# Kernel tuning notes

Measured on AMD Instinct MI355X. Metric: run time of the kernel, lower is better.

Reference implementation:

```python
import jax, jax.numpy as jnp
import numpy as np

N_GEN, N_LOAD, N_OR, N_EX = 10000, 20000, 35000, 35000
N = N_GEN + N_LOAD + N_OR + N_EX  # 100000 objects
E = 1_600_000                      # edges (avg degree 16)
H = 64                             # N_node_hidden
L_HID = 7                          # N_GCN_layers - 1
NEG = 0.1                          # LeakyReLU negative slope
WS = 0.05                          # weight scale


def setup_inputs() -> dict:
    key = jax.random.key(0)
    ks = jax.random.split(key, 32)
    f = lambda i, s: jax.random.normal(ks[i], s, jnp.float32)
    p = lambda i, s: WS * jax.random.normal(ks[i], s, jnp.float32)
    return {
        "x_gen": f(0, (N_GEN, 3)),
        "x_load": f(1, (N_LOAD, 3)),
        "x_or": f(2, (N_OR, 6)),
        "x_ex": f(3, (N_EX, 6)),
        "edge_index": jax.random.randint(ks[4], (2, E), 0, N, jnp.int32),
        "object_ptv": jnp.arange(N, dtype=jnp.int32),
        "W_gen1": p(5, (3, H)), "b_gen1": p(6, (H,)),
        "W_gen2": p(7, (H, H)), "b_gen2": p(8, (H,)),
        "W_load1": p(9, (3, H)), "b_load1": p(10, (H,)),
        "W_load2": p(11, (H, H)), "b_load2": p(12, (H,)),
        "W_or1": p(13, (6, H)), "b_or1": p(14, (H,)),
        "W_or2": p(15, (H, H)), "b_or2": p(16, (H,)),
        "W_ex1": p(17, (6, H)), "b_ex1": p(18, (H,)),
        "W_ex2": p(19, (H, H)), "b_ex2": p(20, (H,)),
        "Wl_h": p(21, (L_HID, H, H)),
        "Wr_h": p(22, (L_HID, H, H)),
        "b_h": p(23, (L_HID, H)),
        "Wl_last": p(24, (H, 1)),
        "Wr_last": p(25, (H, 1)),
        "b_last": p(26, (1,)),
    }


def _encode(x, W1, b1, W2, b2):
    h = jax.nn.leaky_relu(x @ W1 + b1, NEG)
    return jax.nn.leaky_relu(h @ W2 + b2, NEG)


def reference(x_gen, x_load, x_or, x_ex, edge_index, object_ptv,
              W_gen1, b_gen1, W_gen2, b_gen2,
              W_load1, b_load1, W_load2, b_load2,
              W_or1, b_or1, W_or2, b_or2,
              W_ex1, b_ex1, W_ex2, b_ex2,
              Wl_h, Wr_h, b_h, Wl_last, Wr_last, b_last):
    # per-object-type MLP encoders
    xg = _encode(x_gen, W_gen1, b_gen1, W_gen2, b_gen2)
    xl = _encode(x_load, W_load1, b_load1, W_load2, b_load2)
    xo = _encode(x_or, W_or1, b_or1, W_or2, b_or2)
    xe = _encode(x_ex, W_ex1, b_ex1, W_ex2, b_ex2)
    x = jnp.concatenate([xg, xl, xo, xe], axis=0)[object_ptv]  # [N, H]

    src, dst = edge_index[0], edge_index[1]

    def sage(h, Wl, Wr, b):
        # SAGEConv(aggr='add', root_weight=True): lin_l(sum_j h_j) + lin_r(h_i) + b
        agg = jax.ops.segment_sum(h[src], dst, num_segments=N)  # gather + scatter-add
        return agg @ Wl + h @ Wr + b

    def step(h, params):
        Wl, Wr, b = params
        return jax.nn.leaky_relu(sage(h, Wl, Wr, b), NEG), None

    x, _ = jax.lax.scan(step, x, (Wl_h, Wr_h, b_h))
    return jax.nn.sigmoid(sage(x, Wl_last, Wr_last, b_last))  # [N, 1]
```

## Files before the change

kernel.cpp:

```cpp
#include <hip/hip_runtime.h>
#include <math.h>

#define HD 64
#define NEGS 0.1f
#define CHUNK 2048
#define NPART 8

typedef unsigned short u16;
typedef unsigned int u32;

__device__ __forceinline__ float leaky(float v) { return v > 0.f ? v : NEGS * v; }

__device__ __forceinline__ u16 f2bf(float f) {
    union { float f; u32 u; } v; v.f = f;
    u32 r = v.u + 0x7FFFu + ((v.u >> 16) & 1u);
    return (u16)(r >> 16);
}
__device__ __forceinline__ float bf2f(u16 u) {
    union { u32 i; float f; } v; v.i = ((u32)u) << 16; return v.f;
}
__device__ __forceinline__ float bflo(u32 x) {
    union { u32 i; float f; } v; v.i = x << 16; return v.f;
}
__device__ __forceinline__ float bfhi(u32 x) {
    union { u32 i; float f; } v; v.i = x & 0xFFFF0000u; return v.f;
}
__device__ __forceinline__ u32 pack2(float a, float b) {
    return (u32)f2bf(a) | ((u32)f2bf(b) << 16);
}

__global__ void zero_i32(int* __restrict__ p, int n) {
    int i = blockIdx.x * blockDim.x + threadIdx.x;
    int stride = gridDim.x * blockDim.x;
    for (; i < n; i += stride) p[i] = 0;
}

template <int IN>
__global__ void encode_k(const float* __restrict__ x,
                         const float* __restrict__ W1, const float* __restrict__ b1,
                         const float* __restrict__ W2, const float* __restrict__ b2,
                         u16* __restrict__ out, int n) {
    __shared__ float sW2[HD * HD];
    for (int idx = threadIdx.x; idx < HD * HD; idx += blockDim.x) sW2[idx] = W2[idx];
    __syncthreads();
    int wave = threadIdx.x >> 6, lane = threadIdx.x & 63;
    int i = blockIdx.x * 4 + wave;
    if (i >= n) return;
    float h1 = b1[lane];
#pragma unroll
    for (int d = 0; d < IN; ++d) h1 += x[i * IN + d] * W1[d * HD + lane];
    h1 = leaky(h1);
    float h2 = b2[lane];
#pragma unroll
    for (int k = 0; k < HD; ++k) {
        float hk = __shfl(h1, k);
        h2 += hk * sW2[k * HD + lane];
    }
    out[i * HD + lane] = f2bf(leaky(h2));
}

__global__ void gather_bf(const u16* __restrict__ enc, const int* __restrict__ ptv,
                          u16* __restrict__ out, int n) {
    int idx = blockIdx.x * blockDim.x + threadIdx.x;
    int stride = gridDim.x * blockDim.x;
    int total = n * (HD / 8);
    for (; idx < total; idx += stride) {
        int i = idx >> 3, ch = idx & 7;
        ((uint4*)(out + (size_t)i * HD))[ch] =
            ((const uint4*)(enc + (size_t)ptv[i] * HD))[ch];
    }
}

__global__ void __launch_bounds__(256) hist_part(const int* __restrict__ dst,
                                                 int* __restrict__ counts,
                                                 int E_, int part_sz) {
    int part = blockIdx.x & (NPART - 1);
    int slice = blockIdx.x >> 3;
    int nslices = gridDim.x >> 3;
    int lo = part * part_sz, hi = lo + part_sz;
    for (int e = slice * blockDim.x + threadIdx.x; e < E_; e += nslices * blockDim.x) {
        int d = dst[e];
        if (d >= lo && d < hi) atomicAdd(&counts[d], 1);
    }
}

__global__ void scan1(const int* __restrict__ counts, int* __restrict__ bsum, int n) {
    __shared__ int s[256];
    int b = blockIdx.x, t = threadIdx.x;
    int base = b * CHUNK + t * 8;
    int sum = 0;
#pragma unroll
    for (int u = 0; u < 8; ++u) {
        int i = base + u;
        if (i < n) sum += counts[i];
    }
    s[t] = sum;
    __syncthreads();
    for (int off = 128; off > 0; off >>= 1) {
        if (t < off) s[t] += s[t + off];
        __syncthreads();
    }
    if (t == 0) bsum[b] = s[0];
}

__global__ void scan2(int* __restrict__ bsum, int nb, int* __restrict__ row_ptr, int n) {
    if (threadIdx.x == 0 && blockIdx.x == 0) {
        int run = 0;
        for (int b = 0; b < nb; ++b) {
            int v = bsum[b];
            bsum[b] = run;
            run += v;
        }
        row_ptr[n] = run;
    }
}

__global__ void scan3(const int* __restrict__ counts, const int* __restrict__ bsum,
                      int* __restrict__ row_ptr, int* __restrict__ pos, int n) {
    __shared__ int s[256];
    int b = blockIdx.x, t = threadIdx.x;
    int base = b * CHUNK + t * 8;
    int c[8];
    int sum = 0;
#pragma unroll
    for (int u = 0; u < 8; ++u) {
        int i = base + u;
        c[u] = (i < n) ? counts[i] : 0;
        sum += c[u];
    }
    s[t] = sum;
    __syncthreads();
    for (int off = 1; off < 256; off <<= 1) {
        int v = (t >= off) ? s[t - off] : 0;
        __syncthreads();
        s[t] += v;
        __syncthreads();
    }
    int run = bsum[b] + s[t] - sum;
#pragma unroll
    for (int u = 0; u < 8; ++u) {
        int i = base + u;
        if (i < n) {
            row_ptr[i] = run;
            pos[i] = run;
            run += c[u];
        }
    }
}

__global__ void __launch_bounds__(256) scatter_part(const int* __restrict__ src,
                                                    const int* __restrict__ dst,
                                                    int* __restrict__ pos,
                                                    int* __restrict__ col,
                                                    int E_, int part_sz) {
    int part = blockIdx.x & (NPART - 1);
    int slice = blockIdx.x >> 3;
    int nslices = gridDim.x >> 3;
    int lo = part * part_sz, hi = lo + part_sz;
    for (int e = slice * blockDim.x + threadIdx.x; e < E_; e += nslices * blockDim.x) {
        int d = dst[e];
        if (d >= lo && d < hi) {
            int p = atomicAdd(&pos[d], 1);
            col[p] = src[e];
        }
    }
}

__global__ void __launch_bounds__(256) agg_bf(const u16* __restrict__ hin,
                                              u16* __restrict__ agg,
                                              const int* __restrict__ row_ptr,
                                              const int* __restrict__ col, int n) {
    int wid = threadIdx.x >> 6, lane = threadIdx.x & 63;
    int g = lane >> 4, s = lane & 15;
    int wpb = blockDim.x >> 6;
    int stride = gridDim.x * wpb;
    for (int i = blockIdx.x * wpb + wid; i < n; i += stride) {
        int beg = row_ptr[i], end = row_ptr[i + 1];
        int deg = end - beg;
        float4 a0 = make_float4(0.f, 0.f, 0.f, 0.f);
        float4 a1 = make_float4(0.f, 0.f, 0.f, 0.f);
        float4 a2 = make_float4(0.f, 0.f, 0.f, 0.f);
        float4 a3 = make_float4(0.f, 0.f, 0.f, 0.f);
        for (int base = 0; base < deg; base += 64) {
            int m = deg - base;
            if (m > 64) m = 64;
            int cidx = (lane < m) ? col[beg + base + lane] : 0;
            int k = g;
            for (; k + 12 < m; k += 16) {
                int c0 = __shfl(cidx, k);
                int c1 = __shfl(cidx, k + 4);
                int c2 = __shfl(cidx, k + 8);
                int c3 = __shfl(cidx, k + 12);
                uint2 v0 = ((const uint2*)(hin + (size_t)c0 * HD))[s];
                uint2 v1 = ((const uint2*)(hin + (size_t)c1 * HD))[s];
                uint2 v2 = ((const uint2*)(hin + (size_t)c2 * HD))[s];
                uint2 v3 = ((const uint2*)(hin + (size_t)c3 * HD))[s];
                a0.x += bflo(v0.x); a0.y += bfhi(v0.x); a0.z += bflo(v0.y); a0.w += bfhi(v0.y);
                a1.x += bflo(v1.x); a1.y += bfhi(v1.x); a1.z += bflo(v1.y); a1.w += bfhi(v1.y);
                a2.x += bflo(v2.x); a2.y += bfhi(v2.x); a2.z += bflo(v2.y); a2.w += bfhi(v2.y);
                a3.x += bflo(v3.x); a3.y += bfhi(v3.x); a3.z += bflo(v3.y); a3.w += bfhi(v3.y);
            }
            for (; k < m; k += 4) {
                int c0 = __shfl(cidx, k);
                uint2 v0 = ((const uint2*)(hin + (size_t)c0 * HD))[s];
                a0.x += bflo(v0.x); a0.y += bfhi(v0.x); a0.z += bflo(v0.y); a0.w += bfhi(v0.y);
            }
        }
        a0.x += a1.x + a2.x + a3.x;
        a0.y += a1.y + a2.y + a3.y;
        a0.z += a1.z + a2.z + a3.z;
        a0.w += a1.w + a2.w + a3.w;
        a0.x += __shfl_xor(a0.x, 16);
        a0.y += __shfl_xor(a0.y, 16);
        a0.z += __shfl_xor(a0.z, 16);
        a0.w += __shfl_xor(a0.w, 16);
        a0.x += __shfl_xor(a0.x, 32);
        a0.y += __shfl_xor(a0.y, 32);
        a0.z += __shfl_xor(a0.z, 32);
        a0.w += __shfl_xor(a0.w, 32);
        if (g == 0) {
            uint2 w;
            w.x = pack2(a0.x, a0.y);
            w.y = pack2(a0.z, a0.w);
            ((uint2*)(agg + (size_t)i * HD))[s] = w;
        }
    }
}

__global__ void __launch_bounds__(256) sage_gemm_bf(const u16* __restrict__ agg,
                                                    const u16* __restrict__ h,
                                                    u16* __restrict__ hout,
                                                    const float* __restrict__ Wl,
                                                    const float* __restrict__ Wr,
                                                    const float* __restrict__ bias, int n) {
    __shared__ float Ws[128][64];
    __shared__ float Xs[64][132];
    int tid = threadIdx.x;
    for (int idx = tid; idx < 64 * 64; idx += 256) {
        int k = idx >> 6, j = idx & 63;
        Ws[k][j] = Wl[idx];
        Ws[64 + k][j] = Wr[idx];
    }
    int tcol = tid & 15, trow = tid >> 4;
    int j0 = tcol * 4;
    float b0 = bias[j0], b1 = bias[j0 + 1], b2 = bias[j0 + 2], b3 = bias[j0 + 3];
    int ntiles = (n + 63) >> 6;
    for (int t = blockIdx.x; t < ntiles; t += gridDim.x) {
        int base = t << 6;
        __syncthreads();
#pragma unroll
        for (int u = 0; u < 4; ++u) {
            int idx = tid + u * 256;
            int row = idx >> 4, ch = idx & 15;
            int grow = base + row;
            uint4 q = make_uint4(0u, 0u, 0u, 0u);
            if (grow < n) {
                q = (ch < 8) ? ((const uint4*)(agg + (size_t)grow * HD))[ch]
                             : ((const uint4*)(h + (size_t)grow * HD))[ch - 8];
            }
            float* xp = &Xs[row][ch * 8];
            xp[0] = bflo(q.x); xp[1] = bfhi(q.x);
            xp[2] = bflo(q.y); xp[3] = bfhi(q.y);
            xp[4] = bflo(q.z); xp[5] = bfhi(q.z);
            xp[6] = bflo(q.w); xp[7] = bfhi(q.w);
        }
        __syncthreads();
        float acc[4][4];
#pragma unroll
        for (int r = 0; r < 4; ++r)
#pragma unroll
            for (int c = 0; c < 4; ++c) acc[r][c] = 0.f;
#pragma unroll 4
        for (int k4 = 0; k4 < 32; ++k4) {
            int k = k4 * 4;
            float4 x0 = *(const float4*)&Xs[trow][k];
            float4 x1 = *(const float4*)&Xs[trow + 16][k];
            float4 x2 = *(const float4*)&Xs[trow + 32][k];
            float4 x3 = *(const float4*)&Xs[trow + 48][k];
            float4 w0 = *(const float4*)&Ws[k][j0];
            float4 w1 = *(const float4*)&Ws[k + 1][j0];
            float4 w2 = *(const float4*)&Ws[k + 2][j0];
            float4 w3 = *(const float4*)&Ws[k + 3][j0];
            float4 xr[4] = {x0, x1, x2, x3};
#pragma unroll
            for (int r = 0; r < 4; ++r) {
                acc[r][0] += xr[r].x * w0.x + xr[r].y * w1.x + xr[r].z * w2.x + xr[r].w * w3.x;
                acc[r][1] += xr[r].x * w0.y + xr[r].y * w1.y + xr[r].z * w2.y + xr[r].w * w3.y;
                acc[r][2] += xr[r].x * w0.z + xr[r].y * w1.z + xr[r].z * w2.z + xr[r].w * w3.z;
                acc[r][3] += xr[r].x * w0.w + xr[r].y * w1.w + xr[r].z * w2.w + xr[r].w * w3.w;
            }
        }
#pragma unroll
        for (int r = 0; r < 4; ++r) {
            int grow = base + trow + 16 * r;
            if (grow < n) {
                uint2 o;
                o.x = pack2(leaky(acc[r][0] + b0), leaky(acc[r][1] + b1));
                o.y = pack2(leaky(acc[r][2] + b2), leaky(acc[r][3] + b3));
                *(uint2*)(hout + (size_t)grow * HD + j0) = o;
            }
        }
    }
}

__global__ void __launch_bounds__(256) dot_bf(const u16* __restrict__ h,
                                              const float* __restrict__ Wl,
                                              const float* __restrict__ Wr,
                                              float* __restrict__ sb, float* __restrict__ tb,
                                              int n) {
    int wid = threadIdx.x >> 6, lane = threadIdx.x & 63;
    float wl = Wl[lane], wr = Wr[lane];
    int wpb = blockDim.x >> 6;
    int stride = gridDim.x * wpb;
    for (int i = blockIdx.x * wpb + wid; i < n; i += stride) {
        float hv = bf2f(h[(size_t)i * HD + lane]);
        float a = hv * wl;
        float c = hv * wr;
#pragma unroll
        for (int off = 32; off > 0; off >>= 1) {
            a += __shfl_xor(a, off);
            c += __shfl_xor(c, off);
        }
        if (lane == 0) {
            sb[i] = a;
            tb[i] = c;
        }
    }
}

__global__ void __launch_bounds__(256) last_k(const float* __restrict__ sb,
                                              const float* __restrict__ tb,
                                              const int* __restrict__ row_ptr,
                                              const int* __restrict__ col,
                                              const float* __restrict__ b_last,
                                              float* __restrict__ out, int n) {
    float b0 = b_last[0];
    int stride = gridDim.x * blockDim.x;
    for (int i = blockIdx.x * blockDim.x + threadIdx.x; i < n; i += stride) {
        int beg = row_ptr[i], end = row_ptr[i + 1];
        float acc = 0.f;
        for (int k = beg; k < end; ++k) acc += sb[col[k]];
        out[i] = 1.f / (1.f + expf(-(acc + tb[i] + b0)));
    }
}

extern "C" void kernel_launch(void* const* d_in, const int* in_sizes, int n_in,
                              void* d_out, int out_size, void* d_ws, size_t ws_size,
                              hipStream_t stream) {
    const float* x_gen = (const float*)d_in[0];
    const float* x_load = (const float*)d_in[1];
    const float* x_or = (const float*)d_in[2];
    const float* x_ex = (const float*)d_in[3];
    const int* edge = (const int*)d_in[4];
    const int* ptv = (const int*)d_in[5];
    const float* W_gen1 = (const float*)d_in[6];
    const float* b_gen1 = (const float*)d_in[7];
    const float* W_gen2 = (const float*)d_in[8];
    const float* b_gen2 = (const float*)d_in[9];
    const float* W_load1 = (const float*)d_in[10];
    const float* b_load1 = (const float*)d_in[11];
    const float* W_load2 = (const float*)d_in[12];
    const float* b_load2 = (const float*)d_in[13];
    const float* W_or1 = (const float*)d_in[14];
    const float* b_or1 = (const float*)d_in[15];
    const float* W_or2 = (const float*)d_in[16];
    const float* b_or2 = (const float*)d_in[17];
    const float* W_ex1 = (const float*)d_in[18];
    const float* b_ex1 = (const float*)d_in[19];
    const float* W_ex2 = (const float*)d_in[20];
    const float* b_ex2 = (const float*)d_in[21];
    const float* Wl_h = (const float*)d_in[22];
    const float* Wr_h = (const float*)d_in[23];
    const float* b_h = (const float*)d_in[24];
    const float* Wl_last = (const float*)d_in[25];
    const float* Wr_last = (const float*)d_in[26];
    const float* b_last = (const float*)d_in[27];

    int n_gen = in_sizes[0] / 3;
    int n_load = in_sizes[1] / 3;
    int n_or = in_sizes[2] / 6;
    int n_ex = in_sizes[3] / 6;
    int E_ = in_sizes[4] / 2;
    int N_ = in_sizes[5];
    const int* srcv = edge;
    const int* dstv = edge + E_;

    char* ws = (char*)d_ws;
    size_t off = 0;
    auto alloc = [&](size_t bytes) -> void* {
        void* p = ws + off;
        off = (off + bytes + 255) & ~(size_t)255;
        return p;
    };
    u16* enc = (u16*)alloc((size_t)N_ * HD * 2);
    u16* hA = (u16*)alloc((size_t)N_ * HD * 2);
    u16* hB = (u16*)alloc((size_t)N_ * HD * 2);
    int* counts = (int*)alloc((size_t)N_ * 4);
    int* row_ptr = (int*)alloc((size_t)(N_ + 1) * 4);
    int* pos = (int*)alloc((size_t)N_ * 4);
    int* bsum = (int*)alloc(256 * 4);
    int* csr_col = (int*)alloc((size_t)E_ * 4);
    float* sbuf = (float*)alloc((size_t)N_ * 4);
    float* tbuf = (float*)alloc((size_t)N_ * 4);
    u16* agg = enc;
    (void)ws_size;

    int part_sz = (N_ + NPART - 1) / NPART;

    zero_i32<<<256, 256, 0, stream>>>(counts, N_);

    encode_k<3><<<(n_gen + 3) / 4, 256, 0, stream>>>(x_gen, W_gen1, b_gen1, W_gen2, b_gen2,
                                                     enc, n_gen);
    encode_k<3><<<(n_load + 3) / 4, 256, 0, stream>>>(x_load, W_load1, b_load1, W_load2, b_load2,
                                                      enc + (size_t)n_gen * HD, n_load);
    encode_k<6><<<(n_or + 3) / 4, 256, 0, stream>>>(x_or, W_or1, b_or1, W_or2, b_or2,
                                                    enc + (size_t)(n_gen + n_load) * HD, n_or);
    encode_k<6><<<(n_ex + 3) / 4, 256, 0, stream>>>(x_ex, W_ex1, b_ex1, W_ex2, b_ex2,
                                                    enc + (size_t)(n_gen + n_load + n_or) * HD, n_ex);

    gather_bf<<<1024, 256, 0, stream>>>(enc, ptv, hA, N_);

    hist_part<<<2048, 256, 0, stream>>>(dstv, counts, E_, part_sz);
    int nb = (N_ + CHUNK - 1) / CHUNK;
    scan1<<<nb, 256, 0, stream>>>(counts, bsum, N_);
    scan2<<<1, 64, 0, stream>>>(bsum, nb, row_ptr, N_);
    scan3<<<nb, 256, 0, stream>>>(counts, bsum, row_ptr, pos, N_);
    scatter_part<<<2048, 256, 0, stream>>>(srcv, dstv, pos, csr_col, E_, part_sz);

    int ntiles = (N_ + 63) >> 6;
    int ggrid = ntiles < 512 ? ntiles : 512;
    u16* cur = hA;
    u16* nxt = hB;
    for (int l = 0; l < 7; ++l) {
        agg_bf<<<4096, 256, 0, stream>>>(cur, agg, row_ptr, csr_col, N_);
        sage_gemm_bf<<<ggrid, 256, 0, stream>>>(agg, cur, nxt,
                                                Wl_h + (size_t)l * HD * HD,
                                                Wr_h + (size_t)l * HD * HD,
                                                b_h + (size_t)l * HD, N_);
        u16* t = cur;
        cur = nxt;
        nxt = t;
    }
    dot_bf<<<1024, 256, 0, stream>>>(cur, Wl_last, Wr_last, sbuf, tbuf, N_);
    last_k<<<512, 256, 0, stream>>>(sbuf, tbuf, row_ptr, csr_col, b_last,
                                    (float*)d_out, N_);
}
```

Baseline: 817.2 us.

## Fuse neighbor aggregation into the SAGE GEMM kernel per 64-row tile

Replaces the separate aggregation and GEMM kernels with one 512-thread kernel. Each of its 8 wavefronts aggregates neighbor features for 8 rows directly into shared memory, and the block then runs the 64x128 by 128x64 product. This removes the bf16 round trip of the agg buffer through global memory, one launch per layer, and one bf16 rounding of the aggregate. The cost is that the gather, which was spread over 4096 blocks, now runs inside only up to 512 blocks. Latency hiding for the random gathers may therefore drop, and uneven degrees stall whole tiles.

```diff
diff --git a/kernel.cpp b/kernel.cpp
--- a/kernel.cpp
+++ b/kernel.cpp
@@ -166,81 +166,23 @@
     }
 }
 
-__global__ void __launch_bounds__(256) agg_bf(const u16* __restrict__ hin,
-                                              u16* __restrict__ agg,
-                                              const int* __restrict__ row_ptr,
-                                              const int* __restrict__ col, int n) {
-    int wid = threadIdx.x >> 6, lane = threadIdx.x & 63;
-    int g = lane >> 4, s = lane & 15;
-    int wpb = blockDim.x >> 6;
-    int stride = gridDim.x * wpb;
-    for (int i = blockIdx.x * wpb + wid; i < n; i += stride) {
-        int beg = row_ptr[i], end = row_ptr[i + 1];
-        int deg = end - beg;
-        float4 a0 = make_float4(0.f, 0.f, 0.f, 0.f);
-        float4 a1 = make_float4(0.f, 0.f, 0.f, 0.f);
-        float4 a2 = make_float4(0.f, 0.f, 0.f, 0.f);
-        float4 a3 = make_float4(0.f, 0.f, 0.f, 0.f);
-        for (int base = 0; base < deg; base += 64) {
-            int m = deg - base;
-            if (m > 64) m = 64;
-            int cidx = (lane < m) ? col[beg + base + lane] : 0;
-            int k = g;
-            for (; k + 12 < m; k += 16) {
-                int c0 = __shfl(cidx, k);
-                int c1 = __shfl(cidx, k + 4);
-                int c2 = __shfl(cidx, k + 8);
-                int c3 = __shfl(cidx, k + 12);
-                uint2 v0 = ((const uint2*)(hin + (size_t)c0 * HD))[s];
-                uint2 v1 = ((const uint2*)(hin + (size_t)c1 * HD))[s];
-                uint2 v2 = ((const uint2*)(hin + (size_t)c2 * HD))[s];
-                uint2 v3 = ((const uint2*)(hin + (size_t)c3 * HD))[s];
-                a0.x += bflo(v0.x); a0.y += bfhi(v0.x); a0.z += bflo(v0.y); a0.w += bfhi(v0.y);
-                a1.x += bflo(v1.x); a1.y += bfhi(v1.x); a1.z += bflo(v1.y); a1.w += bfhi(v1.y);
-                a2.x += bflo(v2.x); a2.y += bfhi(v2.x); a2.z += bflo(v2.y); a2.w += bfhi(v2.y);
-                a3.x += bflo(v3.x); a3.y += bfhi(v3.x); a3.z += bflo(v3.y); a3.w += bfhi(v3.y);
-            }
-            for (; k < m; k += 4) {
-                int c0 = __shfl(cidx, k);
-                uint2 v0 = ((const uint2*)(hin + (size_t)c0 * HD))[s];
-                a0.x += bflo(v0.x); a0.y += bfhi(v0.x); a0.z += bflo(v0.y); a0.w += bfhi(v0.y);
-            }
-        }
-        a0.x += a1.x + a2.x + a3.x;
-        a0.y += a1.y + a2.y + a3.y;
-        a0.z += a1.z + a2.z + a3.z;
-        a0.w += a1.w + a2.w + a3.w;
-        a0.x += __shfl_xor(a0.x, 16);
-        a0.y += __shfl_xor(a0.y, 16);
-        a0.z += __shfl_xor(a0.z, 16);
-        a0.w += __shfl_xor(a0.w, 16);
-        a0.x += __shfl_xor(a0.x, 32);
-        a0.y += __shfl_xor(a0.y, 32);
-        a0.z += __shfl_xor(a0.z, 32);
-        a0.w += __shfl_xor(a0.w, 32);
-        if (g == 0) {
-            uint2 w;
-            w.x = pack2(a0.x, a0.y);
-            w.y = pack2(a0.z, a0.w);
-            ((uint2*)(agg + (size_t)i * HD))[s] = w;
-        }
-    }
-}
-
-__global__ void __launch_bounds__(256) sage_gemm_bf(const u16* __restrict__ agg,
-                                                    const u16* __restrict__ h,
-                                                    u16* __restrict__ hout,
-                                                    const float* __restrict__ Wl,
-                                                    const float* __restrict__ Wr,
-                                                    const float* __restrict__ bias, int n) {
+__global__ void __launch_bounds__(512) sage_fused(const u16* __restrict__ hin,
+                                                  u16* __restrict__ hout,
+                                                  const int* __restrict__ row_ptr,
+                                                  const int* __restrict__ col,
+                                                  const float* __restrict__ Wl,
+                                                  const float* __restrict__ Wr,
+                                                  const float* __restrict__ bias, int n) {
     __shared__ float Ws[128][64];
     __shared__ float Xs[64][132];
     int tid = threadIdx.x;
-    for (int idx = tid; idx < 64 * 64; idx += 256) {
+    for (int idx = tid; idx < 64 * 64; idx += 512) {
         int k = idx >> 6, j = idx & 63;
         Ws[k][j] = Wl[idx];
         Ws[64 + k][j] = Wr[idx];
     }
+    int wid = tid >> 6, lane = tid & 63;
+    int g = lane >> 4, s = lane & 15;
     int tcol = tid & 15, trow = tid >> 4;
     int j0 = tcol * 4;
     float b0 = bias[j0], b1 = bias[j0 + 1], b2 = bias[j0 + 2], b3 = bias[j0 + 3];
@@ -248,42 +190,84 @@
     for (int t = blockIdx.x; t < ntiles; t += gridDim.x) {
         int base = t << 6;
         __syncthreads();
-#pragma unroll
-        for (int u = 0; u < 4; ++u) {
-            int idx = tid + u * 256;
-            int row = idx >> 4, ch = idx & 15;
+        {
+            int row = tid >> 3, ch = tid & 7;
             int grow = base + row;
             uint4 q = make_uint4(0u, 0u, 0u, 0u);
-            if (grow < n) {
-                q = (ch < 8) ? ((const uint4*)(agg + (size_t)grow * HD))[ch]
-                             : ((const uint4*)(h + (size_t)grow * HD))[ch - 8];
-            }
-            float* xp = &Xs[row][ch * 8];
+            if (grow < n) q = ((const uint4*)(hin + (size_t)grow * HD))[ch];
+            float* xp = &Xs[row][64 + ch * 8];
             xp[0] = bflo(q.x); xp[1] = bfhi(q.x);
             xp[2] = bflo(q.y); xp[3] = bfhi(q.y);
             xp[4] = bflo(q.z); xp[5] = bfhi(q.z);
             xp[6] = bflo(q.w); xp[7] = bfhi(q.w);
         }
+        for (int it = 0; it < 8; ++it) {
+            int r = wid * 8 + it;
+            int grow = base + r;
+            if (grow >= n) break;
+            int beg = row_ptr[grow], end = row_ptr[grow + 1];
+            int deg = end - beg;
+            float4 a0 = make_float4(0.f, 0.f, 0.f, 0.f);
+            float4 a1 = make_float4(0.f, 0.f, 0.f, 0.f);
+            float4 a2 = make_float4(0.f, 0.f, 0.f, 0.f);
+            float4 a3 = make_float4(0.f, 0.f, 0.f, 0.f);
+            for (int bb = 0; bb < deg; bb += 64) {
+                int m = deg - bb;
+                if (m > 64) m = 64;
+                int cidx = (lane < m) ? col[beg + bb + lane] : 0;
+                int k = g;
+                for (; k + 12 < m; k += 16) {
+                    int c0 = __shfl(cidx, k);
+                    int c1 = __shfl(cidx, k + 4);
+                    int c2 = __shfl(cidx, k + 8);
+                    int c3 = __shfl(cidx, k + 12);
+                    uint2 v0 = ((const uint2*)(hin + (size_t)c0 * HD))[s];
+                    uint2 v1 = ((const uint2*)(hin + (size_t)c1 * HD))[s];
+                    uint2 v2 = ((const uint2*)(hin + (size_t)c2 * HD))[s];
+                    uint2 v3 = ((const uint2*)(hin + (size_t)c3 * HD))[s];
+                    a0.x += bflo(v0.x); a0.y += bfhi(v0.x); a0.z += bflo(v0.y); a0.w += bfhi(v0.y);
+                    a1.x += bflo(v1.x); a1.y += bfhi(v1.x); a1.z += bflo(v1.y); a1.w += bfhi(v1.y);
+                    a2.x += bflo(v2.x); a2.y += bfhi(v2.x); a2.z += bflo(v2.y); a2.w += bfhi(v2.y);
+                    a3.x += bflo(v3.x); a3.y += bfhi(v3.x); a3.z += bflo(v3.y); a3.w += bfhi(v3.y);
+                }
+                for (; k < m; k += 4) {
+                    int c0 = __shfl(cidx, k);
+                    uint2 v0 = ((const uint2*)(hin + (size_t)c0 * HD))[s];
+                    a0.x += bflo(v0.x); a0.y += bfhi(v0.x); a0.z += bflo(v0.y); a0.w += bfhi(v0.y);
+                }
+            }
+            a0.x += a1.x + a2.x + a3.x;
+            a0.y += a1.y + a2.y + a3.y;
+            a0.z += a1.z + a2.z + a3.z;
+            a0.w += a1.w + a2.w + a3.w;
+            a0.x += __shfl_xor(a0.x, 16);
+            a0.y += __shfl_xor(a0.y, 16);
+            a0.z += __shfl_xor(a0.z, 16);
+            a0.w += __shfl_xor(a0.w, 16);
+            a0.x += __shfl_xor(a0.x, 32);
+            a0.y += __shfl_xor(a0.y, 32);
+            a0.z += __shfl_xor(a0.z, 32);
+            a0.w += __shfl_xor(a0.w, 32);
+            if (g == 0) *(float4*)&Xs[r][s * 4] = a0;
+        }
         __syncthreads();
-        float acc[4][4];
-#pragma unroll
-        for (int r = 0; r < 4; ++r)
+        float acc[2][4];
+#pragma unroll
+        for (int r = 0; r < 2; ++r)
 #pragma unroll
             for (int c = 0; c < 4; ++c) acc[r][c] = 0.f;
 #pragma unroll 4
         for (int k4 = 0; k4 < 32; ++k4) {
             int k = k4 * 4;
             float4 x0 = *(const float4*)&Xs[trow][k];
-            float4 x1 = *(const float4*)&Xs[trow + 16][k];
-            float4 x2 = *(const float4*)&Xs[trow + 32][k];
-            float4 x3 = *(const float4*)&Xs[trow + 48][k];
+            float4 x1 = *(const float4*)&Xs[trow + 32][k];
             float4 w0 = *(const float4*)&Ws[k][j0];
             float4 w1 = *(const float4*)&Ws[k + 1][j0];
             float4 w2 = *(const float4*)&Ws[k + 2][j0];
             float4 w3 = *(const float4*)&Ws[k + 3][j0];
-            float4 xr[4] = {x0, x1, x2, x3};
-#pragma unroll
-            for (int r = 0; r < 4; ++r) {
+            float4 xr[2] = {x0, x1};
+#pragma unroll
+            for (int r = 0; r < 2; ++r) {
                 acc[r][0] += xr[r].x * w0.x + xr[r].y * w1.x + xr[r].z * w2.x + xr[r].w * w3.x;
                 acc[r][1] += xr[r].x * w0.y + xr[r].y * w1.y + xr[r].z * w2.y + xr[r].w * w3.y;
                 acc[r][2] += xr[r].x * w0.z + xr[r].y * w1.z + xr[r].z * w2.z + xr[r].w * w3.z;
@@ -291,8 +275,8 @@
             }
         }
 #pragma unroll
-        for (int r = 0; r < 4; ++r) {
-            int grow = base + trow + 16 * r;
+        for (int r = 0; r < 2; ++r) {
+            int grow = base + trow + 32 * r;
             if (grow < n) {
                 uint2 o;
                 o.x = pack2(leaky(acc[r][0] + b0), leaky(acc[r][1] + b1));
@@ -402,7 +386,6 @@
     int* csr_col = (int*)alloc((size_t)E_ * 4);
     float* sbuf = (float*)alloc((size_t)N_ * 4);
     float* tbuf = (float*)alloc((size_t)N_ * 4);
-    u16* agg = enc;
     (void)ws_size;
 
     int part_sz = (N_ + NPART - 1) / NPART;
@@ -428,15 +411,14 @@
     scatter_part<<<2048, 256, 0, stream>>>(srcv, dstv, pos, csr_col, E_, part_sz);
 
     int ntiles = (N_ + 63) >> 6;
-    int ggrid = ntiles < 512 ? ntiles : 512;
+    int fgrid = ntiles < 512 ? ntiles : 512;
     u16* cur = hA;
     u16* nxt = hB;
     for (int l = 0; l < 7; ++l) {
-        agg_bf<<<4096, 256, 0, stream>>>(cur, agg, row_ptr, csr_col, N_);
-        sage_gemm_bf<<<ggrid, 256, 0, stream>>>(agg, cur, nxt,
-                                                Wl_h + (size_t)l * HD * HD,
-                                                Wr_h + (size_t)l * HD * HD,
-                                                b_h + (size_t)l * HD, N_);
+        sage_fused<<<fgrid, 512, 0, stream>>>(cur, nxt, row_ptr, csr_col,
+                                              Wl_h + (size_t)l * HD * HD,
+                                              Wr_h + (size_t)l * HD * HD,
+                                              b_h + (size_t)l * HD, N_);
         u16* t = cur;
         cur = nxt;
         nxt = t;
```

Result: slower. 971.0 us (+18.8%).

## Pre-bucket edges by destination partition before histogram and CSR scatter

Applied to the files above, without the earlier changes.

Adds a first pass that splits edges into NPART destination-range buckets, using block-local shared-memory counters and one global atomic per bucket per block. The histogram and scatter kernels then read only their own bucket instead of each scanning all edges NPART times and filtering. This cuts redundant reads of src/dst in the CSR build, at the cost of an extra pass and extra bucket buffers. Bucket capacity is fixed at E/NPART plus a slack, so a skewed destination distribution could overflow a bucket.

```diff
diff --git a/kernel.cpp b/kernel.cpp
--- a/kernel.cpp
+++ b/kernel.cpp
@@ -5,6 +5,7 @@
 #define NEGS 0.1f
 #define CHUNK 2048
 #define NPART 8
+#define BK_SLACK 4096
 
 typedef unsigned short u16;
 typedef unsigned int u32;
@@ -71,17 +72,49 @@
     }
 }
 
-__global__ void __launch_bounds__(256) hist_part(const int* __restrict__ dst,
-                                                 int* __restrict__ counts,
-                                                 int E_, int part_sz) {
-    int part = blockIdx.x & (NPART - 1);
+__global__ void __launch_bounds__(256) bucket1(const int* __restrict__ src,
+                                               const int* __restrict__ dst,
+                                               int* __restrict__ bsrc,
+                                               int* __restrict__ bdst,
+                                               int* __restrict__ bcur,
+                                               int E_, int part_sz, int cap) {
+    __shared__ int lcnt[NPART];
+    __shared__ int lbase[NPART];
+    int tid = threadIdx.x;
+    if (tid < NPART) lcnt[tid] = 0;
+    __syncthreads();
+    int per = (E_ + gridDim.x - 1) / gridDim.x;
+    int s0 = blockIdx.x * per;
+    int s1 = s0 + per;
+    if (s1 > E_) s1 = E_;
+    for (int e = s0 + tid; e < s1; e += 256)
+        atomicAdd(&lcnt[dst[e] / part_sz], 1);
+    __syncthreads();
+    if (tid < NPART) {
+        lbase[tid] = atomicAdd(&bcur[tid], lcnt[tid]);
+        lcnt[tid] = 0;
+    }
+    __syncthreads();
+    for (int e = s0 + tid; e < s1; e += 256) {
+        int d = dst[e];
+        int p = d / part_sz;
+        int off = atomicAdd(&lcnt[p], 1);
+        int slot = p * cap + lbase[p] + off;
+        bsrc[slot] = src[e];
+        bdst[slot] = d;
+    }
+}
+
+__global__ void __launch_bounds__(256) hist_bucket(const int* __restrict__ bdst,
+                                                   const int* __restrict__ bcur,
+                                                   int* __restrict__ counts, int cap) {
+    int p = blockIdx.x & (NPART - 1);
     int slice = blockIdx.x >> 3;
-    int nslices = gridDim.x >> 3;
-    int lo = part * part_sz, hi = lo + part_sz;
-    for (int e = slice * blockDim.x + threadIdx.x; e < E_; e += nslices * blockDim.x) {
-        int d = dst[e];
-        if (d >= lo && d < hi) atomicAdd(&counts[d], 1);
-    }
+    int nsl = gridDim.x >> 3;
+    int cnt = bcur[p];
+    const int* bp = bdst + (size_t)p * cap;
+    for (int e = slice * 256 + threadIdx.x; e < cnt; e += nsl * 256)
+        atomicAdd(&counts[bp[e]], 1);
 }
 
 __global__ void scan1(const int* __restrict__ counts, int* __restrict__ bsum, int n) {
@@ -148,21 +181,21 @@
     }
 }
 
-__global__ void __launch_bounds__(256) scatter_part(const int* __restrict__ src,
-                                                    const int* __restrict__ dst,
-                                                    int* __restrict__ pos,
-                                                    int* __restrict__ col,
-                                                    int E_, int part_sz) {
-    int part = blockIdx.x & (NPART - 1);
+__global__ void __launch_bounds__(256) bucket2(const int* __restrict__ bsrc,
+                                               const int* __restrict__ bdst,
+                                               const int* __restrict__ bcur,
+                                               int* __restrict__ pos,
+                                               int* __restrict__ col, int cap) {
+    int p = blockIdx.x & (NPART - 1);
     int slice = blockIdx.x >> 3;
-    int nslices = gridDim.x >> 3;
-    int lo = part * part_sz, hi = lo + part_sz;
-    for (int e = slice * blockDim.x + threadIdx.x; e < E_; e += nslices * blockDim.x) {
-        int d = dst[e];
-        if (d >= lo && d < hi) {
-            int p = atomicAdd(&pos[d], 1);
-            col[p] = src[e];
-        }
+    int nsl = gridDim.x >> 3;
+    int cnt = bcur[p];
+    const int* bs = bsrc + (size_t)p * cap;
+    const int* bd = bdst + (size_t)p * cap;
+    for (int e = slice * 256 + threadIdx.x; e < cnt; e += nsl * 256) {
+        int d = bd[e];
+        int sl = atomicAdd(&pos[d], 1);
+        col[sl] = bs[e];
     }
 }
 
@@ -402,12 +435,16 @@
     int* csr_col = (int*)alloc((size_t)E_ * 4);
     float* sbuf = (float*)alloc((size_t)N_ * 4);
     float* tbuf = (float*)alloc((size_t)N_ * 4);
+    int part_sz = (N_ + NPART - 1) / NPART;
+    int cap = E_ / NPART + BK_SLACK;
+    int* bsrc = (int*)alloc((size_t)NPART * cap * 4);
+    int* bdst = (int*)alloc((size_t)NPART * cap * 4);
+    int* bcur = (int*)alloc(NPART * 4);
     u16* agg = enc;
     (void)ws_size;
 
-    int part_sz = (N_ + NPART - 1) / NPART;
-
     zero_i32<<<256, 256, 0, stream>>>(counts, N_);
+    zero_i32<<<1, 64, 0, stream>>>(bcur, NPART);
 
     encode_k<3><<<(n_gen + 3) / 4, 256, 0, stream>>>(x_gen, W_gen1, b_gen1, W_gen2, b_gen2,
                                                      enc, n_gen);
@@ -420,12 +457,13 @@
 
     gather_bf<<<1024, 256, 0, stream>>>(enc, ptv, hA, N_);
 
-    hist_part<<<2048, 256, 0, stream>>>(dstv, counts, E_, part_sz);
+    bucket1<<<1024, 256, 0, stream>>>(srcv, dstv, bsrc, bdst, bcur, E_, part_sz, cap);
+    hist_bucket<<<2048, 256, 0, stream>>>(bdst, bcur, counts, cap);
     int nb = (N_ + CHUNK - 1) / CHUNK;
     scan1<<<nb, 256, 0, stream>>>(counts, bsum, N_);
     scan2<<<1, 64, 0, stream>>>(bsum, nb, row_ptr, N_);
     scan3<<<nb, 256, 0, stream>>>(counts, bsum, row_ptr, pos, N_);
-    scatter_part<<<2048, 256, 0, stream>>>(srcv, dstv, pos, csr_col, E_, part_sz);
+    bucket2<<<2048, 256, 0, stream>>>(bsrc, bdst, bcur, pos, csr_col, cap);
 
     int ntiles = (N_ + 63) >> 6;
     int ggrid = ntiles < 512 ? ntiles : 512;
```

New measurement: 835.9 us. 2.3% more time.
